# Optimization experiments

Hardware: AMD Instinct MI355X
Metric: run time of the kernel (lower is better)

## Reference

```python
import jax, jax.numpy as jnp
import numpy as np

WSZ = 8
HEADS = 8
DIM_HEAD = 32
DIM = 256
SCALE = DIM_HEAD ** -0.5


def _ln(x, g, b, eps):
    m = jnp.mean(x, axis=-1, keepdims=True)
    v = jnp.var(x, axis=-1, keepdims=True)
    return (x - m) / jnp.sqrt(v + eps) * g + b


def _dpb(rel, w1, b1, g1, bb1, w2, b2, g2, bb2, w3, b3, g3, bb3, w4, b4):
    h = jax.nn.relu(_ln(rel @ w1 + b1, g1, bb1, 1e-3))
    h = jax.nn.relu(_ln(h @ w2 + b2, g2, bb2, 1e-3))
    h = jax.nn.relu(_ln(h @ w3 + b3, g3, bb3, 1e-3))
    return (h @ w4 + b4)[..., 0]


def setup_inputs() -> dict:
    key = jax.random.key(0)
    ks = jax.random.split(key, 8)
    d4 = DIM // 4
    inp = {
        'x': jax.random.normal(ks[0], (8, 128, 128, DIM), jnp.float32),
        'norm_g': jnp.ones((DIM,), jnp.float32),
        'norm_b': jnp.zeros((DIM,), jnp.float32),
        'w_qkv': jax.random.normal(ks[1], (DIM, 3 * HEADS * DIM_HEAD), jnp.float32) * 0.02,
        'w_out': jax.random.normal(ks[2], (HEADS * DIM_HEAD, DIM), jnp.float32) * 0.02,
        'b_out': jnp.zeros((DIM,), jnp.float32),
        'dpb_w1': jax.random.normal(ks[3], (2, d4), jnp.float32) * 0.02,
        'dpb_b1': jnp.zeros((d4,), jnp.float32),
        'dpb_ln1_g': jnp.ones((d4,), jnp.float32),
        'dpb_ln1_b': jnp.zeros((d4,), jnp.float32),
        'dpb_w2': jax.random.normal(ks[4], (d4, d4), jnp.float32) * 0.02,
        'dpb_b2': jnp.zeros((d4,), jnp.float32),
        'dpb_ln2_g': jnp.ones((d4,), jnp.float32),
        'dpb_ln2_b': jnp.zeros((d4,), jnp.float32),
        'dpb_w3': jax.random.normal(ks[5], (d4, d4), jnp.float32) * 0.02,
        'dpb_b3': jnp.zeros((d4,), jnp.float32),
        'dpb_ln3_g': jnp.ones((d4,), jnp.float32),
        'dpb_ln3_b': jnp.zeros((d4,), jnp.float32),
        'dpb_w4': jax.random.normal(ks[6], (d4, 1), jnp.float32) * 0.02,
        'dpb_b4': jnp.zeros((1,), jnp.float32),
    }
    return inp


def reference(x, norm_g, norm_b, w_qkv, w_out, b_out,
              dpb_w1, dpb_b1, dpb_ln1_g, dpb_ln1_b,
              dpb_w2, dpb_b2, dpb_ln2_g, dpb_ln2_b,
              dpb_w3, dpb_b3, dpb_ln3_g, dpb_ln3_b,
              dpb_w4, dpb_b4):
    B, H, W, D = x.shape
    wsz = WSZ
    nh, nw = H // wsz, W // wsz
    s = wsz * wsz  # tokens per window

    # pre-norm (custom LayerNorm, eps=1e-5)
    xn = _ln(x, norm_g, norm_b, 1e-5)

    # 'short' window partition: b (h s1) (w s2) d -> (b h w) (s1 s2) d
    xw = xn.reshape(B, nh, wsz, nw, wsz, D).transpose(0, 1, 3, 2, 4, 5).reshape(B * nh * nw, s, D)

    # 1x1 conv == dense over channels (no bias)
    qkv = xw @ w_qkv  # (nb, s, 3*inner)
    q, k, v = jnp.split(qkv, 3, axis=-1)
    split = lambda t: t.reshape(t.shape[0], s, HEADS, DIM_HEAD).transpose(0, 2, 1, 3)
    q, k, v = split(q), split(k), split(v)

    sim = jnp.einsum('bhid,bhjd->bhij', q * SCALE, k)  # (nb, h, s, s)

    # dynamic position bias MLP over all relative offsets, gathered by index table
    pos = jnp.arange(-wsz, wsz + 1)
    rel = jnp.stack(jnp.meshgrid(pos, pos, indexing='ij'), axis=-1).reshape(-1, 2).astype(x.dtype)
    biases = _dpb(rel, dpb_w1, dpb_b1, dpb_ln1_g, dpb_ln1_b,
                  dpb_w2, dpb_b2, dpb_ln2_g, dpb_ln2_b,
                  dpb_w3, dpb_b3, dpb_ln3_g, dpb_ln3_b,
                  dpb_w4, dpb_b4)  # ((2w+1)^2,)
    p = jnp.arange(wsz)
    g = jnp.stack(jnp.meshgrid(p, p, indexing='ij'), axis=-1).reshape(-1, 2)
    rp = g[:, None] - g[None, :] + wsz - 1
    idx = rp[..., 0] * (2 * wsz - 1) + rp[..., 1]  # (s, s)
    sim = sim + biases[idx]

    attn = jax.nn.softmax(sim, axis=-1)
    out = jnp.einsum('bhij,bhjd->bhid', attn, v)
    out = out.transpose(0, 2, 1, 3).reshape(B * nh * nw, s, HEADS * DIM_HEAD)

    # 1x1 conv out projection (with bias)
    out = out @ w_out + b_out

    # un-window: (b h w) s1 s2 d -> b (h s1) (w s2) d
    out = out.reshape(B, nh, nw, wsz, wsz, D).transpose(0, 1, 3, 2, 4, 5).reshape(B, H, W, D)
    return out
```

## Files before the change

### kernel.cpp

```cpp
#include <hip/hip_runtime.h>
#include <math.h>

#define ATTN_SCALE 0.17677669529663687f
#define XH_STRIDE 264
#define QK_STRIDE 264
#define VT_STRIDE 72
#define BE_STRIDE 68

typedef __attribute__((ext_vector_type(8))) _Float16 f16x8;
typedef __attribute__((ext_vector_type(4))) _Float16 f16x4;
typedef __attribute__((ext_vector_type(4))) float f32x4;

__device__ __forceinline__ f32x4 mfma16(f16x8 a, f16x8 b, f32x4 c) {
  return __builtin_amdgcn_mfma_f32_16x16x32_f16(a, b, c, 0, 0, 0);
}

__device__ __forceinline__ float wave_sum64(float v) {
#pragma unroll
  for (int m = 1; m < 64; m <<= 1) v += __shfl_xor(v, m, 64);
  return v;
}

__global__ void dpb_kernel(const float* __restrict__ w1, const float* __restrict__ b1,
                           const float* __restrict__ g1, const float* __restrict__ bb1,
                           const float* __restrict__ w2, const float* __restrict__ b2,
                           const float* __restrict__ g2, const float* __restrict__ bb2,
                           const float* __restrict__ w3, const float* __restrict__ b3,
                           const float* __restrict__ g3, const float* __restrict__ bb3,
                           const float* __restrict__ w4, const float* __restrict__ b4,
                           float* __restrict__ biases) {
  const int r = blockIdx.x;
  const int lane = threadIdx.x;
  const float rel0 = (float)(r / 17 - 8);
  const float rel1 = (float)(r % 17 - 8);

  float h = rel0 * w1[lane] + rel1 * w1[64 + lane] + b1[lane];
  {
    const float mean = wave_sum64(h) * (1.f / 64.f);
    const float d = h - mean;
    const float var = wave_sum64(d * d) * (1.f / 64.f);
    h = fmaxf(d * rsqrtf(var + 1e-3f) * g1[lane] + bb1[lane], 0.f);
  }
  float h2 = b2[lane];
  for (int i = 0; i < 64; ++i) h2 += __shfl(h, i, 64) * w2[i * 64 + lane];
  {
    const float mean = wave_sum64(h2) * (1.f / 64.f);
    const float d = h2 - mean;
    const float var = wave_sum64(d * d) * (1.f / 64.f);
    h2 = fmaxf(d * rsqrtf(var + 1e-3f) * g2[lane] + bb2[lane], 0.f);
  }
  float h3 = b3[lane];
  for (int i = 0; i < 64; ++i) h3 += __shfl(h2, i, 64) * w3[i * 64 + lane];
  {
    const float mean = wave_sum64(h3) * (1.f / 64.f);
    const float d = h3 - mean;
    const float var = wave_sum64(d * d) * (1.f / 64.f);
    h3 = fmaxf(d * rsqrtf(var + 1e-3f) * g3[lane] + bb3[lane], 0.f);
  }
  float p = wave_sum64(h3 * w4[lane]);
  if (lane == 0) biases[r] = p + b4[0];
}

__global__ void prep_wqkv(const float* __restrict__ w, _Float16* __restrict__ th,
                          _Float16* __restrict__ tl) {
  const int o = blockIdx.x;
  const int k = threadIdx.x;
  float v = w[k * 768 + o];
  if (o < 256) v *= ATTN_SCALE;
  const _Float16 hi = (_Float16)v;
  th[o * 256 + k] = hi;
  tl[o * 256 + k] = (_Float16)(v - (float)hi);
}

__global__ void prep_wout(const float* __restrict__ w, _Float16* __restrict__ th,
                          _Float16* __restrict__ tl) {
  const int o = blockIdx.x;
  const int k = threadIdx.x;
  const float v = w[k * 256 + o];
  const _Float16 hi = (_Float16)v;
  th[o * 256 + k] = hi;
  tl[o * 256 + k] = (_Float16)(v - (float)hi);
}

__global__ __launch_bounds__(512, 2) void attn_mfma2(
    const float* __restrict__ x, const float* __restrict__ gamma,
    const float* __restrict__ beta,
    const _Float16* __restrict__ wqh, const _Float16* __restrict__ wql,
    const _Float16* __restrict__ woh, const _Float16* __restrict__ wol,
    const float* __restrict__ bout, const float* __restrict__ biases,
    float* __restrict__ out) {
  __shared__ __align__(16) _Float16 xh[64 * XH_STRIDE];
  __shared__ __align__(16) _Float16 Qs[64 * QK_STRIDE];
  __shared__ __align__(16) _Float16 Ks[64 * QK_STRIDE];
  __shared__ __align__(16) _Float16 Vt[256 * VT_STRIDE];
  __shared__ __align__(16) float    Bexp[64 * BE_STRIDE];

  const int tid = threadIdx.x;
  const int lane = tid & 63;
  const int w = tid >> 6;
  const int l15 = lane & 15;
  const int khi = lane >> 4;

  const int wi = blockIdx.x;
  const int bb_ = wi >> 8;
  const int hb = (wi >> 4) & 15;
  const int wb = wi & 15;

  {
    const int t = tid >> 3;
    const int d0 = (tid & 7) * 32;
    const int row = hb * 8 + (t >> 3);
    const int col = wb * 8 + (t & 7);
    const float* gp = x + ((((size_t)bb_ * 128 + row) * 128 + col) * 256 + d0);
    float vv[32];
    float sum = 0.f, ssq = 0.f;
#pragma unroll
    for (int j = 0; j < 8; ++j) {
      const float4 v4 = *(const float4*)(gp + j * 4);
      vv[j * 4 + 0] = v4.x; vv[j * 4 + 1] = v4.y;
      vv[j * 4 + 2] = v4.z; vv[j * 4 + 3] = v4.w;
      sum += v4.x + v4.y + v4.z + v4.w;
      ssq += v4.x * v4.x + v4.y * v4.y + v4.z * v4.z + v4.w * v4.w;
    }
#pragma unroll
    for (int mm = 1; mm < 8; mm <<= 1) {
      sum += __shfl_xor(sum, mm, 64);
      ssq += __shfl_xor(ssq, mm, 64);
    }
    const float mean = sum * (1.f / 256.f);
    const float var = ssq * (1.f / 256.f) - mean * mean;
    const float rstd = rsqrtf(var + 1e-5f);
#pragma unroll
    for (int q = 0; q < 8; ++q) {
      const float4 g4 = *(const float4*)(gamma + d0 + q * 4);
      const float4 b4 = *(const float4*)(beta + d0 + q * 4);
      vv[q * 4 + 0] = (vv[q * 4 + 0] - mean) * rstd * g4.x + b4.x;
      vv[q * 4 + 1] = (vv[q * 4 + 1] - mean) * rstd * g4.y + b4.y;
      vv[q * 4 + 2] = (vv[q * 4 + 2] - mean) * rstd * g4.z + b4.z;
      vv[q * 4 + 3] = (vv[q * 4 + 3] - mean) * rstd * g4.w + b4.w;
    }
#pragma unroll
    for (int q = 0; q < 4; ++q) {
      f16x8 pk;
#pragma unroll
      for (int e = 0; e < 8; ++e) pk[e] = (_Float16)vv[q * 8 + e];
      *(f16x8*)&xh[t * XH_STRIDE + d0 + q * 8] = pk;
    }
  }

#pragma unroll
  for (int j = 0; j < 8; ++j) {
    const int e = tid + 512 * j;
    const int qt = e >> 6, kt = e & 63;
    const int idx = ((qt >> 3) - (kt >> 3) + 7) * 15 + ((qt & 7) - (kt & 7) + 7);
    Bexp[qt * BE_STRIDE + kt] = biases[idx];
  }

  __syncthreads();

  {
    f32x4 acc[6][4];
#pragma unroll
    for (int j = 0; j < 6; ++j)
#pragma unroll
      for (int m = 0; m < 4; ++m) acc[j][m] = (f32x4){0.f, 0.f, 0.f, 0.f};

    const int ko0 = khi * 8;
#pragma unroll
    for (int kt = 0; kt < 8; ++kt) {
      const int ko = kt * 32 + ko0;
      f16x8 a0 = *(const f16x8*)&xh[(0 * 16 + l15) * XH_STRIDE + ko];
      f16x8 a1 = *(const f16x8*)&xh[(1 * 16 + l15) * XH_STRIDE + ko];
      f16x8 a2 = *(const f16x8*)&xh[(2 * 16 + l15) * XH_STRIDE + ko];
      f16x8 a3 = *(const f16x8*)&xh[(3 * 16 + l15) * XH_STRIDE + ko];
#pragma unroll
      for (int j = 0; j < 6; ++j) {
        const int wcol = (w * 6 + j) * 16 + l15;
        const int base = wcol * 256 + ko;
        const f16x8 bh = *(const f16x8*)&wqh[base];
        const f16x8 bl = *(const f16x8*)&wql[base];
        acc[j][0] = mfma16(a0, bh, acc[j][0]); acc[j][0] = mfma16(a0, bl, acc[j][0]);
        acc[j][1] = mfma16(a1, bh, acc[j][1]); acc[j][1] = mfma16(a1, bl, acc[j][1]);
        acc[j][2] = mfma16(a2, bh, acc[j][2]); acc[j][2] = mfma16(a2, bl, acc[j][2]);
        acc[j][3] = mfma16(a3, bh, acc[j][3]); acc[j][3] = mfma16(a3, bl, acc[j][3]);
      }
    }

#pragma unroll
    for (int j = 0; j < 6; ++j) {
      const int wcol = (w * 6 + j) * 16 + l15;
      if (wcol < 256) {
#pragma unroll
        for (int m = 0; m < 4; ++m)
#pragma unroll
          for (int rg = 0; rg < 4; ++rg)
            Qs[(m * 16 + khi * 4 + rg) * QK_STRIDE + wcol] = (_Float16)acc[j][m][rg];
      } else if (wcol < 512) {
#pragma unroll
        for (int m = 0; m < 4; ++m)
#pragma unroll
          for (int rg = 0; rg < 4; ++rg)
            Ks[(m * 16 + khi * 4 + rg) * QK_STRIDE + (wcol - 256)] = (_Float16)acc[j][m][rg];
      } else {
        const int vcol = wcol - 512;
#pragma unroll
        for (int m = 0; m < 4; ++m) {
          f16x4 pv;
#pragma unroll
          for (int rg = 0; rg < 4; ++rg) pv[rg] = (_Float16)acc[j][m][rg];
          *(f16x4*)&Vt[vcol * VT_STRIDE + m * 16 + khi * 4] = pv;
        }
      }
    }
  }

  __syncthreads();

  {
    const int h = w;
    const int hoff = h * 32 + khi * 8;

    f16x8 ka[4], qb[4];
#pragma unroll
    for (int mt = 0; mt < 4; ++mt)
      ka[mt] = *(const f16x8*)&Ks[(mt * 16 + l15) * QK_STRIDE + hoff];
#pragma unroll
    for (int nt = 0; nt < 4; ++nt)
      qb[nt] = *(const f16x8*)&Qs[(nt * 16 + l15) * QK_STRIDE + hoff];

    f32x4 st[4][4];
#pragma unroll
    for (int mt = 0; mt < 4; ++mt)
#pragma unroll
      for (int nt = 0; nt < 4; ++nt) {
        st[mt][nt] = (f32x4){0.f, 0.f, 0.f, 0.f};
        st[mt][nt] = mfma16(ka[mt], qb[nt], st[mt][nt]);
      }

#pragma unroll
    for (int nt = 0; nt < 4; ++nt) {
      const int qrow = (nt * 16 + l15) * BE_STRIDE;
#pragma unroll
      for (int mt = 0; mt < 4; ++mt) {
        const f32x4 bv = *(const f32x4*)&Bexp[qrow + mt * 16 + khi * 4];
        st[mt][nt] = st[mt][nt] + bv;
      }
    }

#pragma unroll
    for (int nt = 0; nt < 4; ++nt) {
      float mx = st[0][nt][0];
#pragma unroll
      for (int mt = 0; mt < 4; ++mt)
#pragma unroll
        for (int rg = 0; rg < 4; ++rg) mx = fmaxf(mx, st[mt][nt][rg]);
      mx = fmaxf(mx, __shfl_xor(mx, 16, 64));
      mx = fmaxf(mx, __shfl_xor(mx, 32, 64));
      float sm = 0.f;
#pragma unroll
      for (int mt = 0; mt < 4; ++mt)
#pragma unroll
        for (int rg = 0; rg < 4; ++rg) {
          const float e = __expf(st[mt][nt][rg] - mx);
          st[mt][nt][rg] = e;
          sm += e;
        }
      sm += __shfl_xor(sm, 16, 64);
      sm += __shfl_xor(sm, 32, 64);
      const float inv = 1.f / sm;
#pragma unroll
      for (int mt = 0; mt < 4; ++mt)
#pragma unroll
        for (int rg = 0; rg < 4; ++rg) st[mt][nt][rg] *= inv;
    }

#pragma unroll
    for (int nt = 0; nt < 4; ++nt) {
      const int qt = nt * 16 + l15;
#pragma unroll
      for (int mt = 0; mt < 4; ++mt) {
        f16x4 pp;
#pragma unroll
        for (int rg = 0; rg < 4; ++rg) pp[rg] = (_Float16)st[mt][nt][rg];
        if (mt < 2)
          *(f16x4*)&Qs[qt * QK_STRIDE + h * 32 + mt * 16 + khi * 4] = pp;
        else
          *(f16x4*)&Ks[qt * QK_STRIDE + h * 32 + (mt - 2) * 16 + khi * 4] = pp;
      }
    }

    f32x4 ot[2][4];
#pragma unroll
    for (int dt = 0; dt < 2; ++dt)
#pragma unroll
      for (int nn = 0; nn < 4; ++nn) ot[dt][nn] = (f32x4){0.f, 0.f, 0.f, 0.f};

#pragma unroll
    for (int kt2 = 0; kt2 < 2; ++kt2) {
      f16x8 va[2], pb[4];
#pragma unroll
      for (int dt = 0; dt < 2; ++dt)
        va[dt] = *(const f16x8*)&Vt[(h * 32 + dt * 16 + l15) * VT_STRIDE + kt2 * 32 + khi * 8];
#pragma unroll
      for (int nn = 0; nn < 4; ++nn) {
        if (kt2 == 0)
          pb[nn] = *(const f16x8*)&Qs[(nn * 16 + l15) * QK_STRIDE + hoff];
        else
          pb[nn] = *(const f16x8*)&Ks[(nn * 16 + l15) * QK_STRIDE + hoff];
      }
#pragma unroll
      for (int dt = 0; dt < 2; ++dt)
#pragma unroll
        for (int nn = 0; nn < 4; ++nn) ot[dt][nn] = mfma16(va[dt], pb[nn], ot[dt][nn]);
    }

#pragma unroll
    for (int nn = 0; nn < 4; ++nn) {
      const int tok = nn * 16 + l15;
#pragma unroll
      for (int dt = 0; dt < 2; ++dt) {
        f16x4 ov;
#pragma unroll
        for (int rg = 0; rg < 4; ++rg) ov[rg] = (_Float16)ot[dt][nn][rg];
        *(f16x4*)&Ks[tok * QK_STRIDE + h * 32 + dt * 16 + khi * 4] = ov;
      }
    }
  }

  __syncthreads();

  {
    f32x4 yacc[2][4];
#pragma unroll
    for (int j = 0; j < 2; ++j)
#pragma unroll
      for (int m = 0; m < 4; ++m) yacc[j][m] = (f32x4){0.f, 0.f, 0.f, 0.f};

    const int ko0 = khi * 8;
#pragma unroll
    for (int kt = 0; kt < 8; ++kt) {
      const int ko = kt * 32 + ko0;
      f16x8 a0 = *(const f16x8*)&Ks[(0 * 16 + l15) * QK_STRIDE + ko];
      f16x8 a1 = *(const f16x8*)&Ks[(1 * 16 + l15) * QK_STRIDE + ko];
      f16x8 a2 = *(const f16x8*)&Ks[(2 * 16 + l15) * QK_STRIDE + ko];
      f16x8 a3 = *(const f16x8*)&Ks[(3 * 16 + l15) * QK_STRIDE + ko];
#pragma unroll
      for (int j = 0; j < 2; ++j) {
        const int oc = (w * 2 + j) * 16 + l15;
        const int base = oc * 256 + ko;
        const f16x8 bh = *(const f16x8*)&woh[base];
        const f16x8 bl = *(const f16x8*)&wol[base];
        yacc[j][0] = mfma16(a0, bh, yacc[j][0]); yacc[j][0] = mfma16(a0, bl, yacc[j][0]);
        yacc[j][1] = mfma16(a1, bh, yacc[j][1]); yacc[j][1] = mfma16(a1, bl, yacc[j][1]);
        yacc[j][2] = mfma16(a2, bh, yacc[j][2]); yacc[j][2] = mfma16(a2, bl, yacc[j][2]);
        yacc[j][3] = mfma16(a3, bh, yacc[j][3]); yacc[j][3] = mfma16(a3, bl, yacc[j][3]);
      }
    }

#pragma unroll
    for (int j = 0; j < 2; ++j) {
      const int oc = (w * 2 + j) * 16 + l15;
      const float bo = bout[oc];
#pragma unroll
      for (int m = 0; m < 4; ++m)
#pragma unroll
        for (int rg = 0; rg < 4; ++rg) {
          const int tok = m * 16 + khi * 4 + rg;
          const int row = hb * 8 + (tok >> 3);
          const int col = wb * 8 + (tok & 7);
          out[(((size_t)bb_ * 128 + row) * 128 + col) * 256 + oc] = yacc[j][m][rg] + bo;
        }
    }
  }
}

extern "C" void kernel_launch(void* const* d_in, const int* in_sizes, int n_in,
                              void* d_out, int out_size, void* d_ws, size_t ws_size,
                              hipStream_t stream) {
  const float* x    = (const float*)d_in[0];
  const float* ng   = (const float*)d_in[1];
  const float* nb   = (const float*)d_in[2];
  const float* wqkv = (const float*)d_in[3];
  const float* wout = (const float*)d_in[4];
  const float* bout = (const float*)d_in[5];
  const float* dw1  = (const float*)d_in[6];
  const float* db1  = (const float*)d_in[7];
  const float* dg1  = (const float*)d_in[8];
  const float* dbb1 = (const float*)d_in[9];
  const float* dw2  = (const float*)d_in[10];
  const float* db2  = (const float*)d_in[11];
  const float* dg2  = (const float*)d_in[12];
  const float* dbb2 = (const float*)d_in[13];
  const float* dw3  = (const float*)d_in[14];
  const float* db3  = (const float*)d_in[15];
  const float* dg3  = (const float*)d_in[16];
  const float* dbb3 = (const float*)d_in[17];
  const float* dw4  = (const float*)d_in[18];
  const float* db4  = (const float*)d_in[19];

  char* ws = (char*)d_ws;
  float* biases  = (float*)ws;
  _Float16* wqh  = (_Float16*)(ws + 2048);
  _Float16* wql  = (_Float16*)(ws + 2048 + 393216);
  _Float16* woh  = (_Float16*)(ws + 2048 + 786432);
  _Float16* wol  = (_Float16*)(ws + 2048 + 917504);

  float* out = (float*)d_out;

  dpb_kernel<<<289, 64, 0, stream>>>(dw1, db1, dg1, dbb1, dw2, db2, dg2, dbb2,
                                     dw3, db3, dg3, dbb3, dw4, db4, biases);
  prep_wqkv<<<768, 256, 0, stream>>>(wqkv, wqh, wql);
  prep_wout<<<256, 256, 0, stream>>>(wout, woh, wol);
  attn_mfma2<<<2048, 512, 0, stream>>>(x, ng, nb, wqh, wql, woh, wol, bout, biases, out);
}
```

Measured before the change: 552.6 us.

## Split head processing into two passes with XOR-swizzled shared memory

```diff
diff --git a/kernel.cpp b/kernel.cpp
--- a/kernel.cpp
+++ b/kernel.cpp
@@ -2,10 +2,6 @@
 #include <math.h>
 
 #define ATTN_SCALE 0.17677669529663687f
-#define XH_STRIDE 264
-#define QK_STRIDE 264
-#define VT_STRIDE 72
-#define BE_STRIDE 68
 
 typedef __attribute__((ext_vector_type(8))) _Float16 f16x8;
 typedef __attribute__((ext_vector_type(4))) _Float16 f16x4;
@@ -13,6 +9,19 @@
 
 __device__ __forceinline__ f32x4 mfma16(f16x8 a, f16x8 b, f32x4 c) {
   return __builtin_amdgcn_mfma_f32_16x16x32_f16(a, b, c, 0, 0, 0);
+}
+
+__device__ __forceinline__ int SX(int r, int c) {
+  int b = (r << 9) + (c << 1);
+  return (b ^ ((r & 7) << 4)) >> 1;
+}
+__device__ __forceinline__ int SV(int r, int c) {
+  int b = (r << 7) + (c << 1);
+  return (b ^ ((r & 7) << 4)) >> 1;
+}
+__device__ __forceinline__ int SO(int r, int c) {
+  int b = (r << 8) + (c << 1);
+  return (b ^ ((r & 7) << 4)) >> 1;
 }
 
 __device__ __forceinline__ float wave_sum64(float v) {
@@ -61,6 +70,12 @@
   if (lane == 0) biases[r] = p + b4[0];
 }
 
+__global__ void expand_bias(const float* __restrict__ biases, float* __restrict__ bexp) {
+  const int qt = blockIdx.x, kt = threadIdx.x;
+  const int idx = ((qt >> 3) - (kt >> 3) + 7) * 15 + ((qt & 7) - (kt & 7) + 7);
+  bexp[qt * 64 + kt] = biases[idx];
+}
+
 __global__ void prep_wqkv(const float* __restrict__ w, _Float16* __restrict__ th,
                           _Float16* __restrict__ tl) {
   const int o = blockIdx.x;
@@ -82,18 +97,17 @@
   tl[o * 256 + k] = (_Float16)(v - (float)hi);
 }
 
-__global__ __launch_bounds__(512, 2) void attn_mfma2(
+__global__ __launch_bounds__(512, 4) void attn_mfma3(
     const float* __restrict__ x, const float* __restrict__ gamma,
     const float* __restrict__ beta,
     const _Float16* __restrict__ wqh, const _Float16* __restrict__ wql,
     const _Float16* __restrict__ woh, const _Float16* __restrict__ wol,
-    const float* __restrict__ bout, const float* __restrict__ biases,
+    const float* __restrict__ bout, const float* __restrict__ bexp,
     float* __restrict__ out) {
-  __shared__ __align__(16) _Float16 xh[64 * XH_STRIDE];
-  __shared__ __align__(16) _Float16 Qs[64 * QK_STRIDE];
-  __shared__ __align__(16) _Float16 Ks[64 * QK_STRIDE];
-  __shared__ __align__(16) _Float16 Vt[256 * VT_STRIDE];
-  __shared__ __align__(16) float    Bexp[64 * BE_STRIDE];
+  __shared__ __align__(16) _Float16 smem[40960];
+  _Float16* xh = smem;
+  _Float16* qk = smem + 16384;
+  _Float16* vo = smem + 32768;
 
   const int tid = threadIdx.x;
   const int lane = tid & 63;
@@ -144,233 +158,210 @@
       f16x8 pk;
 #pragma unroll
       for (int e = 0; e < 8; ++e) pk[e] = (_Float16)vv[q * 8 + e];
-      *(f16x8*)&xh[t * XH_STRIDE + d0 + q * 8] = pk;
-    }
-  }
-
-#pragma unroll
-  for (int j = 0; j < 8; ++j) {
-    const int e = tid + 512 * j;
-    const int qt = e >> 6, kt = e & 63;
-    const int idx = ((qt >> 3) - (kt >> 3) + 7) * 15 + ((qt & 7) - (kt & 7) + 7);
-    Bexp[qt * BE_STRIDE + kt] = biases[idx];
-  }
+      *(f16x8*)&xh[SX(t, d0 + q * 8)] = pk;
+    }
+  }
+
+  f32x4 yacc[2][4];
+#pragma unroll
+  for (int j = 0; j < 2; ++j)
+#pragma unroll
+    for (int m = 0; m < 4; ++m) yacc[j][m] = (f32x4){0.f, 0.f, 0.f, 0.f};
 
   __syncthreads();
 
-  {
-    f32x4 acc[6][4];
-#pragma unroll
-    for (int j = 0; j < 6; ++j)
-#pragma unroll
-      for (int m = 0; m < 4; ++m) acc[j][m] = (f32x4){0.f, 0.f, 0.f, 0.f};
-
-    const int ko0 = khi * 8;
-#pragma unroll
-    for (int kt = 0; kt < 8; ++kt) {
-      const int ko = kt * 32 + ko0;
-      f16x8 a0 = *(const f16x8*)&xh[(0 * 16 + l15) * XH_STRIDE + ko];
-      f16x8 a1 = *(const f16x8*)&xh[(1 * 16 + l15) * XH_STRIDE + ko];
-      f16x8 a2 = *(const f16x8*)&xh[(2 * 16 + l15) * XH_STRIDE + ko];
-      f16x8 a3 = *(const f16x8*)&xh[(3 * 16 + l15) * XH_STRIDE + ko];
-#pragma unroll
-      for (int j = 0; j < 6; ++j) {
-        const int wcol = (w * 6 + j) * 16 + l15;
-        const int base = wcol * 256 + ko;
-        const f16x8 bh = *(const f16x8*)&wqh[base];
-        const f16x8 bl = *(const f16x8*)&wql[base];
-        acc[j][0] = mfma16(a0, bh, acc[j][0]); acc[j][0] = mfma16(a0, bl, acc[j][0]);
-        acc[j][1] = mfma16(a1, bh, acc[j][1]); acc[j][1] = mfma16(a1, bl, acc[j][1]);
-        acc[j][2] = mfma16(a2, bh, acc[j][2]); acc[j][2] = mfma16(a2, bl, acc[j][2]);
-        acc[j][3] = mfma16(a3, bh, acc[j][3]); acc[j][3] = mfma16(a3, bl, acc[j][3]);
-      }
-    }
-
-#pragma unroll
-    for (int j = 0; j < 6; ++j) {
-      const int wcol = (w * 6 + j) * 16 + l15;
-      if (wcol < 256) {
-#pragma unroll
-        for (int m = 0; m < 4; ++m)
-#pragma unroll
-          for (int rg = 0; rg < 4; ++rg)
-            Qs[(m * 16 + khi * 4 + rg) * QK_STRIDE + wcol] = (_Float16)acc[j][m][rg];
-      } else if (wcol < 512) {
-#pragma unroll
-        for (int m = 0; m < 4; ++m)
-#pragma unroll
-          for (int rg = 0; rg < 4; ++rg)
-            Ks[(m * 16 + khi * 4 + rg) * QK_STRIDE + (wcol - 256)] = (_Float16)acc[j][m][rg];
-      } else {
-        const int vcol = wcol - 512;
-#pragma unroll
-        for (int m = 0; m < 4; ++m) {
-          f16x4 pv;
-#pragma unroll
-          for (int rg = 0; rg < 4; ++rg) pv[rg] = (_Float16)acc[j][m][rg];
-          *(f16x4*)&Vt[vcol * VT_STRIDE + m * 16 + khi * 4] = pv;
+  const f32x4 zz = (f32x4){0.f, 0.f, 0.f, 0.f};
+
+  for (int p = 0; p < 2; ++p) {
+    {
+      f32x4 acc[3][4];
+#pragma unroll
+      for (int jj = 0; jj < 3; ++jj)
+#pragma unroll
+        for (int m = 0; m < 4; ++m) acc[jj][m] = zz;
+
+      int gbase[3];
+#pragma unroll
+      for (int jj = 0; jj < 3; ++jj) {
+        const int t = w * 3 + jj;
+        const int kind = t >> 3, sub = t & 7;
+        gbase[jj] = (kind * 256 + p * 128 + sub * 16 + l15) * 256;
+      }
+      const int ko0 = khi * 8;
+#pragma unroll
+      for (int kt = 0; kt < 8; ++kt) {
+        const int ko = kt * 32 + ko0;
+        const f16x8 a0 = *(const f16x8*)&xh[SX(0 * 16 + l15, ko)];
+        const f16x8 a1 = *(const f16x8*)&xh[SX(1 * 16 + l15, ko)];
+        const f16x8 a2 = *(const f16x8*)&xh[SX(2 * 16 + l15, ko)];
+        const f16x8 a3 = *(const f16x8*)&xh[SX(3 * 16 + l15, ko)];
+#pragma unroll
+        for (int jj = 0; jj < 3; ++jj) {
+          const f16x8 bh = *(const f16x8*)&wqh[gbase[jj] + ko];
+          const f16x8 bl = *(const f16x8*)&wql[gbase[jj] + ko];
+          acc[jj][0] = mfma16(a0, bh, acc[jj][0]); acc[jj][0] = mfma16(a0, bl, acc[jj][0]);
+          acc[jj][1] = mfma16(a1, bh, acc[jj][1]); acc[jj][1] = mfma16(a1, bl, acc[jj][1]);
+          acc[jj][2] = mfma16(a2, bh, acc[jj][2]); acc[jj][2] = mfma16(a2, bl, acc[jj][2]);
+          acc[jj][3] = mfma16(a3, bh, acc[jj][3]); acc[jj][3] = mfma16(a3, bl, acc[jj][3]);
         }
       }
-    }
-  }
-
-  __syncthreads();
-
-  {
-    const int h = w;
-    const int hoff = h * 32 + khi * 8;
-
-    f16x8 ka[4], qb[4];
-#pragma unroll
-    for (int mt = 0; mt < 4; ++mt)
-      ka[mt] = *(const f16x8*)&Ks[(mt * 16 + l15) * QK_STRIDE + hoff];
-#pragma unroll
-    for (int nt = 0; nt < 4; ++nt)
-      qb[nt] = *(const f16x8*)&Qs[(nt * 16 + l15) * QK_STRIDE + hoff];
-
-    f32x4 st[4][4];
-#pragma unroll
-    for (int mt = 0; mt < 4; ++mt)
-#pragma unroll
-      for (int nt = 0; nt < 4; ++nt) {
-        st[mt][nt] = (f32x4){0.f, 0.f, 0.f, 0.f};
-        st[mt][nt] = mfma16(ka[mt], qb[nt], st[mt][nt]);
-      }
-
-#pragma unroll
-    for (int nt = 0; nt < 4; ++nt) {
-      const int qrow = (nt * 16 + l15) * BE_STRIDE;
-#pragma unroll
-      for (int mt = 0; mt < 4; ++mt) {
-        const f32x4 bv = *(const f32x4*)&Bexp[qrow + mt * 16 + khi * 4];
-        st[mt][nt] = st[mt][nt] + bv;
-      }
-    }
-
-#pragma unroll
-    for (int nt = 0; nt < 4; ++nt) {
-      float mx = st[0][nt][0];
-#pragma unroll
-      for (int mt = 0; mt < 4; ++mt)
-#pragma unroll
-        for (int rg = 0; rg < 4; ++rg) mx = fmaxf(mx, st[mt][nt][rg]);
-      mx = fmaxf(mx, __shfl_xor(mx, 16, 64));
-      mx = fmaxf(mx, __shfl_xor(mx, 32, 64));
-      float sm = 0.f;
-#pragma unroll
-      for (int mt = 0; mt < 4; ++mt)
-#pragma unroll
-        for (int rg = 0; rg < 4; ++rg) {
-          const float e = __expf(st[mt][nt][rg] - mx);
-          st[mt][nt][rg] = e;
-          sm += e;
+#pragma unroll
+      for (int jj = 0; jj < 3; ++jj) {
+        const int t = w * 3 + jj;
+        const int kind = t >> 3, sub = t & 7;
+        if (kind == 0) {
+#pragma unroll
+          for (int m = 0; m < 4; ++m)
+#pragma unroll
+            for (int rg = 0; rg < 4; ++rg)
+              qk[SX(m * 16 + khi * 4 + rg, sub * 16 + l15)] = (_Float16)acc[jj][m][rg];
+        } else if (kind == 1) {
+#pragma unroll
+          for (int m = 0; m < 4; ++m)
+#pragma unroll
+            for (int rg = 0; rg < 4; ++rg)
+              qk[SX(m * 16 + khi * 4 + rg, 128 + sub * 16 + l15)] = (_Float16)acc[jj][m][rg];
+        } else {
+#pragma unroll
+          for (int m = 0; m < 4; ++m) {
+            f16x4 pv;
+#pragma unroll
+            for (int rg = 0; rg < 4; ++rg) pv[rg] = (_Float16)acc[jj][m][rg];
+            *(f16x4*)&vo[SV(sub * 16 + l15, m * 16 + khi * 4)] = pv;
+          }
         }
-      sm += __shfl_xor(sm, 16, 64);
-      sm += __shfl_xor(sm, 32, 64);
-      const float inv = 1.f / sm;
-#pragma unroll
-      for (int mt = 0; mt < 4; ++mt)
-#pragma unroll
-        for (int rg = 0; rg < 4; ++rg) st[mt][nt][rg] *= inv;
-    }
-
-#pragma unroll
-    for (int nt = 0; nt < 4; ++nt) {
-      const int qt = nt * 16 + l15;
-#pragma unroll
-      for (int mt = 0; mt < 4; ++mt) {
-        f16x4 pp;
-#pragma unroll
-        for (int rg = 0; rg < 4; ++rg) pp[rg] = (_Float16)st[mt][nt][rg];
-        if (mt < 2)
-          *(f16x4*)&Qs[qt * QK_STRIDE + h * 32 + mt * 16 + khi * 4] = pp;
-        else
-          *(f16x4*)&Ks[qt * QK_STRIDE + h * 32 + (mt - 2) * 16 + khi * 4] = pp;
-      }
-    }
-
-    f32x4 ot[2][4];
-#pragma unroll
-    for (int dt = 0; dt < 2; ++dt)
-#pragma unroll
-      for (int nn = 0; nn < 4; ++nn) ot[dt][nn] = (f32x4){0.f, 0.f, 0.f, 0.f};
-
-#pragma unroll
-    for (int kt2 = 0; kt2 < 2; ++kt2) {
-      f16x8 va[2], pb[4];
+      }
+    }
+    __syncthreads();
+
+    {
+      const int hl = w >> 1, qh = w & 1;
+      f16x8 ka[4], qb[2];
+      f32x4 bias[2][4];
+#pragma unroll
+      for (int kt = 0; kt < 4; ++kt)
+        ka[kt] = *(const f16x8*)&qk[SX(kt * 16 + l15, 128 + hl * 32 + khi * 8)];
+#pragma unroll
+      for (int n = 0; n < 2; ++n)
+        qb[n] = *(const f16x8*)&qk[SX((qh * 2 + n) * 16 + l15, hl * 32 + khi * 8)];
+#pragma unroll
+      for (int n = 0; n < 2; ++n)
+#pragma unroll
+        for (int kt = 0; kt < 4; ++kt)
+          bias[n][kt] = *(const f32x4*)&bexp[(qh * 32 + n * 16 + l15) * 64 + kt * 16 + khi * 4];
+      __syncthreads();
+
+      f32x4 st[4][2];
+#pragma unroll
+      for (int kt = 0; kt < 4; ++kt)
+#pragma unroll
+        for (int n = 0; n < 2; ++n)
+          st[kt][n] = mfma16(ka[kt], qb[n], bias[n][kt]);
+
+#pragma unroll
+      for (int n = 0; n < 2; ++n) {
+        float mx = st[0][n][0];
+#pragma unroll
+        for (int kt = 0; kt < 4; ++kt)
+#pragma unroll
+          for (int rg = 0; rg < 4; ++rg) mx = fmaxf(mx, st[kt][n][rg]);
+        mx = fmaxf(mx, __shfl_xor(mx, 16, 64));
+        mx = fmaxf(mx, __shfl_xor(mx, 32, 64));
+        float sm = 0.f;
+#pragma unroll
+        for (int kt = 0; kt < 4; ++kt)
+#pragma unroll
+          for (int rg = 0; rg < 4; ++rg) {
+            const float e = __expf(st[kt][n][rg] - mx);
+            st[kt][n][rg] = e;
+            sm += e;
+          }
+        sm += __shfl_xor(sm, 16, 64);
+        sm += __shfl_xor(sm, 32, 64);
+        const float inv = 1.f / sm;
+#pragma unroll
+        for (int kt = 0; kt < 4; ++kt)
+#pragma unroll
+          for (int rg = 0; rg < 4; ++rg) st[kt][n][rg] *= inv;
+      }
+
+#pragma unroll
+      for (int n = 0; n < 2; ++n)
+#pragma unroll
+        for (int kt = 0; kt < 4; ++kt) {
+          f16x4 pp;
+#pragma unroll
+          for (int rg = 0; rg < 4; ++rg) pp[rg] = (_Float16)st[kt][n][rg];
+          *(f16x4*)&qk[SX(qh * 32 + n * 16 + l15, hl * 64 + kt * 16 + khi * 4)] = pp;
+        }
+
+      f32x4 ot[2][2];
 #pragma unroll
       for (int dt = 0; dt < 2; ++dt)
-        va[dt] = *(const f16x8*)&Vt[(h * 32 + dt * 16 + l15) * VT_STRIDE + kt2 * 32 + khi * 8];
-#pragma unroll
-      for (int nn = 0; nn < 4; ++nn) {
-        if (kt2 == 0)
-          pb[nn] = *(const f16x8*)&Qs[(nn * 16 + l15) * QK_STRIDE + hoff];
-        else
-          pb[nn] = *(const f16x8*)&Ks[(nn * 16 + l15) * QK_STRIDE + hoff];
-      }
-#pragma unroll
-      for (int dt = 0; dt < 2; ++dt)
-#pragma unroll
-        for (int nn = 0; nn < 4; ++nn) ot[dt][nn] = mfma16(va[dt], pb[nn], ot[dt][nn]);
-    }
-
-#pragma unroll
-    for (int nn = 0; nn < 4; ++nn) {
-      const int tok = nn * 16 + l15;
-#pragma unroll
-      for (int dt = 0; dt < 2; ++dt) {
-        f16x4 ov;
-#pragma unroll
-        for (int rg = 0; rg < 4; ++rg) ov[rg] = (_Float16)ot[dt][nn][rg];
-        *(f16x4*)&Ks[tok * QK_STRIDE + h * 32 + dt * 16 + khi * 4] = ov;
-      }
-    }
-  }
-
-  __syncthreads();
-
-  {
-    f32x4 yacc[2][4];
-#pragma unroll
-    for (int j = 0; j < 2; ++j)
-#pragma unroll
-      for (int m = 0; m < 4; ++m) yacc[j][m] = (f32x4){0.f, 0.f, 0.f, 0.f};
-
-    const int ko0 = khi * 8;
-#pragma unroll
-    for (int kt = 0; kt < 8; ++kt) {
-      const int ko = kt * 32 + ko0;
-      f16x8 a0 = *(const f16x8*)&Ks[(0 * 16 + l15) * QK_STRIDE + ko];
-      f16x8 a1 = *(const f16x8*)&Ks[(1 * 16 + l15) * QK_STRIDE + ko];
-      f16x8 a2 = *(const f16x8*)&Ks[(2 * 16 + l15) * QK_STRIDE + ko];
-      f16x8 a3 = *(const f16x8*)&Ks[(3 * 16 + l15) * QK_STRIDE + ko];
-#pragma unroll
-      for (int j = 0; j < 2; ++j) {
-        const int oc = (w * 2 + j) * 16 + l15;
-        const int base = oc * 256 + ko;
-        const f16x8 bh = *(const f16x8*)&woh[base];
-        const f16x8 bl = *(const f16x8*)&wol[base];
-        yacc[j][0] = mfma16(a0, bh, yacc[j][0]); yacc[j][0] = mfma16(a0, bl, yacc[j][0]);
-        yacc[j][1] = mfma16(a1, bh, yacc[j][1]); yacc[j][1] = mfma16(a1, bl, yacc[j][1]);
-        yacc[j][2] = mfma16(a2, bh, yacc[j][2]); yacc[j][2] = mfma16(a2, bl, yacc[j][2]);
-        yacc[j][3] = mfma16(a3, bh, yacc[j][3]); yacc[j][3] = mfma16(a3, bl, yacc[j][3]);
-      }
-    }
-
-#pragma unroll
-    for (int j = 0; j < 2; ++j) {
-      const int oc = (w * 2 + j) * 16 + l15;
-      const float bo = bout[oc];
-#pragma unroll
-      for (int m = 0; m < 4; ++m)
-#pragma unroll
-        for (int rg = 0; rg < 4; ++rg) {
-          const int tok = m * 16 + khi * 4 + rg;
-          const int row = hb * 8 + (tok >> 3);
-          const int col = wb * 8 + (tok & 7);
-          out[(((size_t)bb_ * 128 + row) * 128 + col) * 256 + oc] = yacc[j][m][rg] + bo;
+#pragma unroll
+        for (int n = 0; n < 2; ++n) ot[dt][n] = zz;
+#pragma unroll
+      for (int k2 = 0; k2 < 2; ++k2) {
+        const f16x8 va0 = *(const f16x8*)&vo[SV(hl * 32 + 0 * 16 + l15, k2 * 32 + khi * 8)];
+        const f16x8 va1 = *(const f16x8*)&vo[SV(hl * 32 + 1 * 16 + l15, k2 * 32 + khi * 8)];
+        const f16x8 pb0 = *(const f16x8*)&qk[SX(qh * 32 + 0 * 16 + l15, hl * 64 + k2 * 32 + khi * 8)];
+        const f16x8 pb1 = *(const f16x8*)&qk[SX(qh * 32 + 1 * 16 + l15, hl * 64 + k2 * 32 + khi * 8)];
+        ot[0][0] = mfma16(va0, pb0, ot[0][0]);
+        ot[0][1] = mfma16(va0, pb1, ot[0][1]);
+        ot[1][0] = mfma16(va1, pb0, ot[1][0]);
+        ot[1][1] = mfma16(va1, pb1, ot[1][1]);
+      }
+      __syncthreads();
+
+#pragma unroll
+      for (int n = 0; n < 2; ++n)
+#pragma unroll
+        for (int dt = 0; dt < 2; ++dt) {
+          f16x4 ov;
+#pragma unroll
+          for (int rg = 0; rg < 4; ++rg) ov[rg] = (_Float16)ot[dt][n][rg];
+          *(f16x4*)&vo[SO(qh * 32 + n * 16 + l15, hl * 32 + dt * 16 + khi * 4)] = ov;
         }
     }
+    __syncthreads();
+
+    {
+#pragma unroll
+      for (int kt = 0; kt < 4; ++kt) {
+        const int ko = kt * 32 + khi * 8;
+        const f16x8 a0 = *(const f16x8*)&vo[SO(0 * 16 + l15, ko)];
+        const f16x8 a1 = *(const f16x8*)&vo[SO(1 * 16 + l15, ko)];
+        const f16x8 a2 = *(const f16x8*)&vo[SO(2 * 16 + l15, ko)];
+        const f16x8 a3 = *(const f16x8*)&vo[SO(3 * 16 + l15, ko)];
+#pragma unroll
+        for (int j = 0; j < 2; ++j) {
+          const int oc = (w * 2 + j) * 16 + l15;
+          const int base = oc * 256 + p * 128 + ko;
+          const f16x8 bh = *(const f16x8*)&woh[base];
+          const f16x8 bl = *(const f16x8*)&wol[base];
+          yacc[j][0] = mfma16(a0, bh, yacc[j][0]); yacc[j][0] = mfma16(a0, bl, yacc[j][0]);
+          yacc[j][1] = mfma16(a1, bh, yacc[j][1]); yacc[j][1] = mfma16(a1, bl, yacc[j][1]);
+          yacc[j][2] = mfma16(a2, bh, yacc[j][2]); yacc[j][2] = mfma16(a2, bl, yacc[j][2]);
+          yacc[j][3] = mfma16(a3, bh, yacc[j][3]); yacc[j][3] = mfma16(a3, bl, yacc[j][3]);
+        }
+      }
+    }
+    __syncthreads();
+  }
+
+#pragma unroll
+  for (int j = 0; j < 2; ++j) {
+    const int oc = (w * 2 + j) * 16 + l15;
+    const float bo = bout[oc];
+#pragma unroll
+    for (int m = 0; m < 4; ++m)
+#pragma unroll
+      for (int rg = 0; rg < 4; ++rg) {
+        const int tok = m * 16 + khi * 4 + rg;
+        const int row = hb * 8 + (tok >> 3);
+        const int col = wb * 8 + (tok & 7);
+        out[(((size_t)bb_ * 128 + row) * 128 + col) * 256 + oc] = yacc[j][m][rg] + bo;
+      }
   }
 }
 
@@ -404,12 +395,14 @@
   _Float16* wql  = (_Float16*)(ws + 2048 + 393216);
   _Float16* woh  = (_Float16*)(ws + 2048 + 786432);
   _Float16* wol  = (_Float16*)(ws + 2048 + 917504);
+  float* bexp    = (float*)(ws + 1050624);
 
   float* out = (float*)d_out;
 
   dpb_kernel<<<289, 64, 0, stream>>>(dw1, db1, dg1, dbb1, dw2, db2, dg2, dbb2,
                                      dw3, db3, dg3, dbb3, dw4, db4, biases);
+  expand_bias<<<64, 64, 0, stream>>>(biases, bexp);
   prep_wqkv<<<768, 256, 0, stream>>>(wqkv, wqh, wql);
   prep_wout<<<256, 256, 0, stream>>>(wout, woh, wol);
-  attn_mfma2<<<2048, 512, 0, stream>>>(x, ng, nb, wqh, wql, woh, wol, bout, biases, out);
-}
+  attn_mfma3<<<2048, 512, 0, stream>>>(x, ng, nb, wqh, wql, woh, wol, bout, bexp, out);
+}
```

Result: slower. 913.4 us (+65.3%).
